# Performance work log

Hardware: AMD Instinct MI355X
Metric: run time of the kernel (lower is better)

The kernel has to match this reference:

```python
import jax, jax.numpy as jnp
import numpy as np

B, T, I, H, O = 128, 512, 256, 512, 256


def setup_inputs() -> dict:
    key = jax.random.key(0)
    ks = jax.random.split(key, 20)
    s_i = 1.0 / np.sqrt(I)
    s_h = 1.0 / np.sqrt(H)
    inp = {
        "x": jax.random.normal(ks[0], (B, T, I), dtype=jnp.float32),
        "Wix_w": jax.random.normal(ks[1], (H, I), dtype=jnp.float32) * s_i,
        "Wix_b": jax.random.normal(ks[2], (H,), dtype=jnp.float32) * s_i,
        "Wih_w": jax.random.normal(ks[3], (H, H), dtype=jnp.float32) * s_h,
        "Wih_b": jax.random.normal(ks[4], (H,), dtype=jnp.float32) * s_h,
        "bi": jnp.zeros((H,), dtype=jnp.float32),
        "Wfx_w": jax.random.normal(ks[5], (H, I), dtype=jnp.float32) * s_i,
        "Wfx_b": jax.random.normal(ks[6], (H,), dtype=jnp.float32) * s_i,
        "Wfh_w": jax.random.normal(ks[7], (H, H), dtype=jnp.float32) * s_h,
        "Wfh_b": jax.random.normal(ks[8], (H,), dtype=jnp.float32) * s_h,
        "bf": jnp.zeros((H,), dtype=jnp.float32),
        "Wgx_w": jax.random.normal(ks[9], (H, I), dtype=jnp.float32) * s_i,
        "Wgx_b": jax.random.normal(ks[10], (H,), dtype=jnp.float32) * s_i,
        "Wgh_w": jax.random.normal(ks[11], (H, H), dtype=jnp.float32) * s_h,
        "Wgh_b": jax.random.normal(ks[12], (H,), dtype=jnp.float32) * s_h,
        "bg": jnp.zeros((H,), dtype=jnp.float32),
        "Wox_w": jax.random.normal(ks[13], (H, I), dtype=jnp.float32) * s_i,
        "Wox_b": jax.random.normal(ks[14], (H,), dtype=jnp.float32) * s_i,
        "Woh_w": jax.random.normal(ks[15], (H, H), dtype=jnp.float32) * s_h,
        "Woh_b": jax.random.normal(ks[16], (H,), dtype=jnp.float32) * s_h,
        "bo": jnp.zeros((H,), dtype=jnp.float32),
        "Wph_w": jax.random.normal(ks[17], (O, H), dtype=jnp.float32) * s_h,
        "Wph_b": jax.random.normal(ks[18], (O,), dtype=jnp.float32) * s_h,
        "bp": jnp.zeros((O,), dtype=jnp.float32),
    }
    return inp


def reference(x, Wix_w, Wix_b, Wih_w, Wih_b, bi,
              Wfx_w, Wfx_b, Wfh_w, Wfh_b, bf,
              Wgx_w, Wgx_b, Wgh_w, Wgh_b, bg,
              Wox_w, Wox_b, Woh_w, Woh_b, bo,
              Wph_w, Wph_b, bp):
    batch = x.shape[0]
    h0 = jnp.zeros((batch, Wih_w.shape[0]), dtype=x.dtype)
    c0 = jnp.zeros_like(h0)

    # Precompute all input projections across time in 4 big GEMMs
    # (same math as per-step Linear calls, just batched over t).
    ix = jnp.einsum('bti,hi->bth', x, Wix_w) + Wix_b + bi
    fx = jnp.einsum('bti,hi->bth', x, Wfx_w) + Wfx_b + bf
    gx = jnp.einsum('bti,hi->bth', x, Wgx_w) + Wgx_b + bg
    ox = jnp.einsum('bti,hi->bth', x, Wox_w) + Wox_b + bo

    def step(carry, xt):
        h, c = carry
        ixt, fxt, gxt, oxt = xt
        i = jax.nn.sigmoid(ixt + h @ Wih_w.T + Wih_b)
        f = jax.nn.sigmoid(fxt + h @ Wfh_w.T + Wfh_b)
        g = jnp.tanh(gxt + h @ Wgh_w.T + Wgh_b)
        o = jax.nn.sigmoid(oxt + h @ Woh_w.T + Woh_b)
        c_new = g * i + c * f
        h_new = jnp.tanh(c_new) * o
        p = h_new @ Wph_w.T + Wph_b + bp
        y = jax.nn.softmax(p, axis=1)
        return (h_new, c_new), y

    # scan over time: [T, B, H] layout
    xs = (jnp.swapaxes(ix, 0, 1), jnp.swapaxes(fx, 0, 1),
          jnp.swapaxes(gx, 0, 1), jnp.swapaxes(ox, 0, 1))
    _, ys = jax.lax.scan(step, (h0, c0), xs)
    return jnp.swapaxes(ys, 0, 1)  # [B, T, O]
```

## Files before the change

kernel.cpp:

```cpp
#include <hip/hip_runtime.h>
#include <hip/hip_bf16.h>
#include <math.h>

#define B_  128
#define T_  512
#define I_  256
#define H_  512
#define O_  256
#define NP  2048
#define BT  65536
#define HB  65536

struct PrepArgs {
    const float* Whw[4];
    const float* Wxw[4];
    const float* Wxb[4];
    const float* Whb[4];
    const float* bg[4];
    const float* Wph_w;
    const float* Wph_b;
    const float* bp;
    float* Wt; float* Wg; float* WgT; float* WphT;
    float* xb; float* hb; float* pb;
};

#define PREP_TOTAL (1048576 + 524288 + 524288 + 131072 + 2048 + 2048 + 256)

__global__ __launch_bounds__(256) void k_prep(PrepArgs a) {
    int idx = blockIdx.x * 256 + threadIdx.x;
    if (idx >= PREP_TOTAL) return;
    int q = idx;
    if (q < 1048576) {
        int k = q >> 11, n = q & 2047;
        int g = n & 3, h = n >> 2;
        a.Wt[q] = a.Whw[g][h * H_ + k];
        return;
    }
    q -= 1048576;
    if (q < 524288) {
        int n = q >> 8, i = q & 255;
        int g = n & 3, h = n >> 2;
        a.Wg[q] = a.Wxw[g][h * I_ + i];
        return;
    }
    q -= 524288;
    if (q < 524288) {
        int i = q >> 11, n = q & 2047;
        int g = n & 3, h = n >> 2;
        a.WgT[q] = a.Wxw[g][h * I_ + i];
        return;
    }
    q -= 524288;
    if (q < 131072) {
        int h = q >> 8, o = q & 255;
        a.WphT[q] = a.Wph_w[o * H_ + h];
        return;
    }
    q -= 131072;
    if (q < 2048) {
        int g = q & 3, h = q >> 2;
        a.xb[q] = a.Wxb[g][h] + a.bg[g][h];
        return;
    }
    q -= 2048;
    if (q < 2048) {
        int g = q & 3, h = q >> 2;
        a.hb[q] = a.Whb[g][h];
        return;
    }
    q -= 2048;
    a.pb[q] = a.Wph_b[q] + a.bp[q];
}

__global__ __launch_bounds__(256) void k_transpose(const float* __restrict__ x,
                                                   float* __restrict__ xT2) {
    __shared__ float lds[32][33];
    int tid = threadIdx.x;
    int tx = tid & 31, ty = tid >> 5;
    int j0 = blockIdx.x * 32;
    int i0 = blockIdx.y * 32;
    int t  = j0 >> 7;
    int b0 = j0 & 127;
#pragma unroll
    for (int rr = 0; rr < 4; ++rr) {
        int jj = ty + rr * 8;
        lds[jj][tx] = x[((size_t)(b0 + jj) * T_ + t) * I_ + i0 + tx];
    }
    __syncthreads();
#pragma unroll
    for (int rr = 0; rr < 4; ++rr) {
        int ii = ty + rr * 8;
        xT2[(size_t)(i0 + ii) * BT + j0 + tx] = lds[tx][ii];
    }
}

__global__ __launch_bounds__(256, 1) void k_xgemm(const float* __restrict__ A,
                                                  const float* __restrict__ Bm,
                                                  const float* __restrict__ bias,
                                                  float* __restrict__ C) {
    __shared__ float As[16][128];
    __shared__ float Bs[16][128];
    int tid = threadIdx.x;
    int tx = tid & 15, ty = tid >> 4;
    int m0 = blockIdx.y * 128, j0 = blockIdx.x * 128;
    float acc[8][8];
#pragma unroll
    for (int i = 0; i < 8; ++i)
#pragma unroll
        for (int j = 0; j < 8; ++j) acc[i][j] = 0.f;

    for (int kt = 0; kt < I_; kt += 16) {
#pragma unroll
        for (int pp = 0; pp < 2; ++pp) {
            int p = tid + pp * 256;
            int row = p >> 2, kq = (p & 3) << 2;
            float4 av = *(const float4*)&A[(size_t)(m0 + row) * I_ + kt + kq];
            As[kq + 0][row] = av.x; As[kq + 1][row] = av.y;
            As[kq + 2][row] = av.z; As[kq + 3][row] = av.w;
        }
#pragma unroll
        for (int pp = 0; pp < 2; ++pp) {
            int p = tid + pp * 256;
            int krow = p >> 5, c4 = (p & 31) << 2;
            *(float4*)&Bs[krow][c4] =
                *(const float4*)&Bm[(size_t)(kt + krow) * BT + j0 + c4];
        }
        __syncthreads();
#pragma unroll
        for (int k = 0; k < 16; ++k) {
            float a[8], b[8];
            *(float4*)&a[0] = *(const float4*)&As[k][ty * 4];
            *(float4*)&a[4] = *(const float4*)&As[k][64 + ty * 4];
            *(float4*)&b[0] = *(const float4*)&Bs[k][tx * 4];
            *(float4*)&b[4] = *(const float4*)&Bs[k][64 + tx * 4];
#pragma unroll
            for (int i = 0; i < 8; ++i)
#pragma unroll
                for (int j = 0; j < 8; ++j) acc[i][j] += a[i] * b[j];
        }
        __syncthreads();
    }
#pragma unroll
    for (int i = 0; i < 8; ++i) {
        int mrow = (i < 4) ? (ty * 4 + i) : (64 + ty * 4 + (i - 4));
        int m = m0 + mrow;
        float bv = bias[m];
        float4 v0 = {acc[i][0] + bv, acc[i][1] + bv, acc[i][2] + bv, acc[i][3] + bv};
        float4 v1 = {acc[i][4] + bv, acc[i][5] + bv, acc[i][6] + bv, acc[i][7] + bv};
        *(float4*)&C[(size_t)m * BT + j0 + tx * 4] = v0;
        *(float4*)&C[(size_t)m * BT + j0 + 64 + tx * 4] = v1;
    }
}

__device__ inline float sigm(float v) { return 1.f / (1.f + expf(-v)); }

template <bool USE_XP>
__global__ __launch_bounds__(256, 1) void k_step(const float* __restrict__ Wt,
                                                 const float* __restrict__ WgT,
                                                 const float* __restrict__ xp,
                                                 const float* __restrict__ xT2,
                                                 const float* __restrict__ xb,
                                                 const float* __restrict__ hb,
                                                 float* __restrict__ hist,
                                                 float* __restrict__ cT,
                                                 int t) {
    __shared__ float red[4][16][64];
    int tid = threadIdx.x;
    int wave = tid >> 6, lane = tid & 63;
    int nt = blockIdx.x >> 1, bh = blockIdx.x & 1;
    int n0 = nt * 16, b0 = bh * 64;
    int b = b0 + lane;

    const float* hrow = hist + (size_t)t * HB;
    float acc[16];
#pragma unroll
    for (int j = 0; j < 16; ++j) acc[j] = 0.f;

    {
        int k0 = wave * 128;
        const float* hp = hrow + (size_t)k0 * B_ + b;
        const float* wp = Wt + (size_t)k0 * NP + n0;
        float hv[8];
#pragma unroll
        for (int u = 0; u < 8; ++u) hv[u] = hp[u * B_];
        for (int kb = 0; kb < 128; kb += 8) {
            float hn[8];
            if (kb + 8 < 128) {
                const float* hp2 = hp + (size_t)(kb + 8) * B_;
#pragma unroll
                for (int u = 0; u < 8; ++u) hn[u] = hp2[u * B_];
            }
#pragma unroll
            for (int u = 0; u < 8; ++u) {
                const float* w = wp + (size_t)(kb + u) * NP;
                float h0 = hv[u];
#pragma unroll
                for (int j = 0; j < 4; ++j) {
                    float4 wv = *(const float4*)(w + j * 4);
                    acc[j * 4 + 0] += h0 * wv.x;
                    acc[j * 4 + 1] += h0 * wv.y;
                    acc[j * 4 + 2] += h0 * wv.z;
                    acc[j * 4 + 3] += h0 * wv.w;
                }
            }
#pragma unroll
            for (int u = 0; u < 8; ++u) hv[u] = hn[u];
        }
    }
    if (!USE_XP) {
        int i0 = wave * 64;
        const float* xpp = xT2 + (size_t)i0 * BT + (size_t)t * B_ + b;
        const float* wp  = WgT + (size_t)i0 * NP + n0;
#pragma unroll 4
        for (int ii = 0; ii < 64; ++ii) {
            float xv = xpp[(size_t)ii * BT];
            const float* w = wp + (size_t)ii * NP;
#pragma unroll
            for (int j = 0; j < 4; ++j) {
                float4 wv = *(const float4*)(w + j * 4);
                acc[j * 4 + 0] += xv * wv.x;
                acc[j * 4 + 1] += xv * wv.y;
                acc[j * 4 + 2] += xv * wv.z;
                acc[j * 4 + 3] += xv * wv.w;
            }
        }
    }
#pragma unroll
    for (int j = 0; j < 16; ++j) red[wave][j][lane] = acc[j];
    __syncthreads();

    int b_l = tid & 63, h_i = tid >> 6;
    int n = n0 + h_i * 4;
    int h = nt * 4 + h_i;
    int bb = b0 + b_l;
    float pre[4];
#pragma unroll
    for (int g = 0; g < 4; ++g) {
        int j = h_i * 4 + g;
        pre[g] = red[0][j][b_l] + red[1][j][b_l] + red[2][j][b_l] + red[3][j][b_l];
        pre[g] += hb[n + g];
        if (USE_XP)
            pre[g] += xp[(size_t)(n + g) * BT + (size_t)t * B_ + bb];
        else
            pre[g] += xb[n + g];
    }
    float iv = sigm(pre[0]);
    float fv = sigm(pre[1]);
    float gv = tanhf(pre[2]);
    float ov = sigm(pre[3]);
    float c  = cT[h * B_ + bb];
    float cn = gv * iv + c * fv;
    cT[h * B_ + bb] = cn;
    hist[(size_t)(t + 1) * HB + h * B_ + bb] = tanhf(cn) * ov;
}

__global__ __launch_bounds__(256, 1) void k_outproj(const float* __restrict__ WphT,
                                                    const float* __restrict__ pb,
                                                    const float* __restrict__ hist,
                                                    float* __restrict__ pT) {
    __shared__ float red[4][16][64];
    int tid = threadIdx.x;
    int wave = tid >> 6, lane = tid & 63;
    int t = blockIdx.y;
    int ot = blockIdx.x >> 1, bh = blockIdx.x & 1;
    int o0 = ot * 16, b0 = bh * 64;
    int b = b0 + lane;

    const float* hrow = hist + (size_t)(t + 1) * HB;
    float acc[16];
#pragma unroll
    for (int j = 0; j < 16; ++j) acc[j] = 0.f;

    int k0 = wave * 128;
    const float* hp = hrow + (size_t)k0 * B_ + b;
    const float* wp = WphT + (size_t)k0 * O_ + o0;
    float hv[8];
#pragma unroll
    for (int u = 0; u < 8; ++u) hv[u] = hp[u * B_];
    for (int kb = 0; kb < 128; kb += 8) {
        float hn[8];
        if (kb + 8 < 128) {
            const float* hp2 = hp + (size_t)(kb + 8) * B_;
#pragma unroll
            for (int u = 0; u < 8; ++u) hn[u] = hp2[u * B_];
        }
#pragma unroll
        for (int u = 0; u < 8; ++u) {
            const float* w = wp + (size_t)(kb + u) * O_;
            float h0 = hv[u];
#pragma unroll
            for (int j = 0; j < 4; ++j) {
                float4 wv = *(const float4*)(w + j * 4);
                acc[j * 4 + 0] += h0 * wv.x;
                acc[j * 4 + 1] += h0 * wv.y;
                acc[j * 4 + 2] += h0 * wv.z;
                acc[j * 4 + 3] += h0 * wv.w;
            }
        }
#pragma unroll
        for (int u = 0; u < 8; ++u) hv[u] = hn[u];
    }
#pragma unroll
    for (int j = 0; j < 16; ++j) red[wave][j][lane] = acc[j];
    __syncthreads();

    int b_l = tid & 63, oi = tid >> 6;
    int bb = b0 + b_l;
#pragma unroll
    for (int g = 0; g < 4; ++g) {
        int j = oi * 4 + g;
        int o = o0 + j;
        float v = red[0][j][b_l] + red[1][j][b_l] + red[2][j][b_l] + red[3][j][b_l] + pb[o];
        pT[(size_t)t * (O_ * B_) + (size_t)o * B_ + bb] = v;
    }
}

__global__ __launch_bounds__(256, 1) void k_softmax(const float* __restrict__ pT,
                                                    float* __restrict__ out) {
    __shared__ float sm[32][257];
    __shared__ float rmax[32][8];
    __shared__ float rsum[32][8];
    int tid = threadIdx.x;
    int t = blockIdx.x >> 2, bq = blockIdx.x & 3;
    int b0 = bq * 32;
    const float* src = pT + (size_t)t * (O_ * B_);

#pragma unroll 4
    for (int it = 0; it < 32; ++it) {
        int idx = it * 256 + tid;
        int o = idx >> 5, b_l = idx & 31;
        sm[b_l][o] = src[(size_t)o * B_ + b0 + b_l];
    }
    __syncthreads();

    int b_l = tid >> 3, oc = tid & 7;
    float m = -3.4e38f;
#pragma unroll 4
    for (int oo = 0; oo < 32; ++oo) m = fmaxf(m, sm[b_l][oc * 32 + oo]);
    rmax[b_l][oc] = m;
    __syncthreads();
    float mm = rmax[b_l][0];
#pragma unroll
    for (int c = 1; c < 8; ++c) mm = fmaxf(mm, rmax[b_l][c]);

    float s = 0.f;
#pragma unroll 4
    for (int oo = 0; oo < 32; ++oo) s += expf(sm[b_l][oc * 32 + oo] - mm);
    rsum[b_l][oc] = s;
    __syncthreads();
    float st = 0.f;
#pragma unroll
    for (int c = 0; c < 8; ++c) st += rsum[b_l][c];
    float inv = 1.f / st;

    int bb = b0 + b_l;
    float* dst = out + ((size_t)bb * T_ + t) * O_ + oc * 32;
#pragma unroll 4
    for (int oo = 0; oo < 32; ++oo)
        dst[oo] = expf(sm[b_l][oc * 32 + oo] - mm) * inv;
}

extern "C" void kernel_launch(void* const* d_in, const int* in_sizes, int n_in,
                              void* d_out, int out_size, void* d_ws, size_t ws_size,
                              hipStream_t stream) {
    const float* x = (const float*)d_in[0];

    float* ws = (float*)d_ws;
    size_t off = 0;
    auto alloc = [&](size_t n) { float* p = ws + off; off += n; return p; };

    float* hist = alloc((size_t)513 * HB);
    float* cT   = alloc(HB);
    float* Wt   = alloc((size_t)512 * NP);
    float* Wg   = alloc((size_t)NP * I_);
    float* WgT  = alloc((size_t)I_ * NP);
    float* WphT = alloc((size_t)H_ * O_);
    float* xb   = alloc(NP);
    float* hb   = alloc(NP);
    float* pb   = alloc(O_);
    float* xT2  = alloc((size_t)I_ * BT);
    size_t baseBytes = off * sizeof(float);
    size_t xpBytes   = (size_t)NP * BT * sizeof(float);

    bool useXp = (ws_size >= baseBytes + xpBytes);
    float* xp = ws + off;
    float* pT = xT2;

    if (ws_size < baseBytes) return;

    hipMemsetAsync(hist, 0, HB * sizeof(float), stream);
    hipMemsetAsync(cT, 0, HB * sizeof(float), stream);

    PrepArgs pa;
    for (int g = 0; g < 4; ++g) {
        pa.Wxw[g] = (const float*)d_in[1 + 5 * g];
        pa.Wxb[g] = (const float*)d_in[2 + 5 * g];
        pa.Whw[g] = (const float*)d_in[3 + 5 * g];
        pa.Whb[g] = (const float*)d_in[4 + 5 * g];
        pa.bg[g]  = (const float*)d_in[5 + 5 * g];
    }
    pa.Wph_w = (const float*)d_in[21];
    pa.Wph_b = (const float*)d_in[22];
    pa.bp    = (const float*)d_in[23];
    pa.Wt = Wt; pa.Wg = Wg; pa.WgT = WgT; pa.WphT = WphT;
    pa.xb = xb; pa.hb = hb; pa.pb = pb;

    k_prep<<<(PREP_TOTAL + 255) / 256, 256, 0, stream>>>(pa);
    k_transpose<<<dim3(BT / 32, I_ / 32), 256, 0, stream>>>(x, xT2);

    if (useXp)
        k_xgemm<<<dim3(BT / 128, NP / 128), 256, 0, stream>>>(Wg, xT2, xb, xp);

    for (int t = 0; t < T_; ++t) {
        if (useXp)
            k_step<true><<<256, 256, 0, stream>>>(Wt, WgT, xp, xT2, xb, hb, hist, cT, t);
        else
            k_step<false><<<256, 256, 0, stream>>>(Wt, WgT, xp, xT2, xb, hb, hist, cT, t);
    }

    k_outproj<<<dim3(32, T_), 256, 0, stream>>>(WphT, pb, hist, pT);
    k_softmax<<<T_ * 4, 256, 0, stream>>>(pT, (float*)d_out);
}
```

Measured before the change: 17.03 ms.

## Replace per-timestep launches with persistent scan kernel using grid barrier

Swaps the 512 per-step kernel launches for one persistent kernel of 256 blocks. Blocks stay resident across time steps and synchronise through a global atomic counter per step. Each block's recurrent weight slice now lives in LDS, and the cell state is kept in registers instead of global memory. This removes launch overhead and repeated weight reloads from global memory, but relies on all 256 blocks being co-resident and on a spin barrier whose timeout could silently break correctness.

```diff
diff --git a/kernel.cpp b/kernel.cpp
--- a/kernel.cpp
+++ b/kernel.cpp
@@ -10,6 +10,7 @@
 #define NP  2048
 #define BT  65536
 #define HB  65536
+#define NBLK 256
 
 struct PrepArgs {
     const float* Whw[4];
@@ -155,103 +156,144 @@
 __device__ inline float sigm(float v) { return 1.f / (1.f + expf(-v)); }
 
 template <bool USE_XP>
-__global__ __launch_bounds__(256, 1) void k_step(const float* __restrict__ Wt,
+__global__ __launch_bounds__(512, 2) void k_scan(const float* __restrict__ Wt,
                                                  const float* __restrict__ WgT,
                                                  const float* __restrict__ xp,
                                                  const float* __restrict__ xT2,
                                                  const float* __restrict__ xb,
                                                  const float* __restrict__ hb,
                                                  float* __restrict__ hist,
-                                                 float* __restrict__ cT,
-                                                 int t) {
-    __shared__ float red[4][16][64];
+                                                 int* __restrict__ bar) {
+    __shared__ float wlds[512][16];
+    __shared__ float wxlds[256][16];
+    __shared__ float red[8][16][64];
+
     int tid = threadIdx.x;
     int wave = tid >> 6, lane = tid & 63;
     int nt = blockIdx.x >> 1, bh = blockIdx.x & 1;
     int n0 = nt * 16, b0 = bh * 64;
+
+    for (int p = tid; p < 2048; p += 512) {
+        int k = p >> 2, q = (p & 3) << 2;
+        *(float4*)&wlds[k][q] = *(const float4*)&Wt[(size_t)k * NP + n0 + q];
+    }
+    if (!USE_XP) {
+        for (int p = tid; p < 1024; p += 512) {
+            int i = p >> 2, q = (p & 3) << 2;
+            *(float4*)&wxlds[i][q] = *(const float4*)&WgT[(size_t)i * NP + n0 + q];
+        }
+    }
+
+    int h_i = tid >> 6, b_l = tid & 63;
+    float c_reg = 0.f;
+    float hbv[4] = {0, 0, 0, 0}, xbv[4] = {0, 0, 0, 0};
+    if (tid < 256) {
+#pragma unroll
+        for (int g = 0; g < 4; ++g) {
+            hbv[g] = hb[n0 + h_i * 4 + g];
+            if (!USE_XP) xbv[g] = xb[n0 + h_i * 4 + g];
+        }
+    }
+    __syncthreads();
+
     int b = b0 + lane;
-
-    const float* hrow = hist + (size_t)t * HB;
-    float acc[16];
-#pragma unroll
-    for (int j = 0; j < 16; ++j) acc[j] = 0.f;
-
-    {
-        int k0 = wave * 128;
-        const float* hp = hrow + (size_t)k0 * B_ + b;
-        const float* wp = Wt + (size_t)k0 * NP + n0;
+    int kc = wave * 64;
+
+    bool dead = false;
+    for (int t = 0; t < T_; ++t) {
+        const float* hp = hist + (size_t)t * HB + (size_t)kc * B_ + b;
+        float acc[16];
+#pragma unroll
+        for (int j = 0; j < 16; ++j) acc[j] = 0.f;
         float hv[8];
 #pragma unroll
         for (int u = 0; u < 8; ++u) hv[u] = hp[u * B_];
-        for (int kb = 0; kb < 128; kb += 8) {
+        for (int kb = 0; kb < 64; kb += 8) {
             float hn[8];
-            if (kb + 8 < 128) {
+            if (kb + 8 < 64) {
                 const float* hp2 = hp + (size_t)(kb + 8) * B_;
 #pragma unroll
                 for (int u = 0; u < 8; ++u) hn[u] = hp2[u * B_];
             }
 #pragma unroll
             for (int u = 0; u < 8; ++u) {
-                const float* w = wp + (size_t)(kb + u) * NP;
+                int k = kc + kb + u;
                 float h0 = hv[u];
 #pragma unroll
-                for (int j = 0; j < 4; ++j) {
-                    float4 wv = *(const float4*)(w + j * 4);
-                    acc[j * 4 + 0] += h0 * wv.x;
-                    acc[j * 4 + 1] += h0 * wv.y;
-                    acc[j * 4 + 2] += h0 * wv.z;
-                    acc[j * 4 + 3] += h0 * wv.w;
+                for (int j4 = 0; j4 < 4; ++j4) {
+                    float4 wv = *(const float4*)&wlds[k][j4 * 4];
+                    acc[j4 * 4 + 0] += h0 * wv.x;
+                    acc[j4 * 4 + 1] += h0 * wv.y;
+                    acc[j4 * 4 + 2] += h0 * wv.z;
+                    acc[j4 * 4 + 3] += h0 * wv.w;
                 }
             }
 #pragma unroll
             for (int u = 0; u < 8; ++u) hv[u] = hn[u];
         }
-    }
-    if (!USE_XP) {
-        int i0 = wave * 64;
-        const float* xpp = xT2 + (size_t)i0 * BT + (size_t)t * B_ + b;
-        const float* wp  = WgT + (size_t)i0 * NP + n0;
+        if (!USE_XP) {
+            int ic = wave * 32;
+            const float* xpp = xT2 + (size_t)ic * BT + (size_t)t * B_ + b;
 #pragma unroll 4
-        for (int ii = 0; ii < 64; ++ii) {
-            float xv = xpp[(size_t)ii * BT];
-            const float* w = wp + (size_t)ii * NP;
-#pragma unroll
-            for (int j = 0; j < 4; ++j) {
-                float4 wv = *(const float4*)(w + j * 4);
-                acc[j * 4 + 0] += xv * wv.x;
-                acc[j * 4 + 1] += xv * wv.y;
-                acc[j * 4 + 2] += xv * wv.z;
-                acc[j * 4 + 3] += xv * wv.w;
-            }
-        }
-    }
-#pragma unroll
-    for (int j = 0; j < 16; ++j) red[wave][j][lane] = acc[j];
-    __syncthreads();
-
-    int b_l = tid & 63, h_i = tid >> 6;
-    int n = n0 + h_i * 4;
-    int h = nt * 4 + h_i;
-    int bb = b0 + b_l;
-    float pre[4];
-#pragma unroll
-    for (int g = 0; g < 4; ++g) {
-        int j = h_i * 4 + g;
-        pre[g] = red[0][j][b_l] + red[1][j][b_l] + red[2][j][b_l] + red[3][j][b_l];
-        pre[g] += hb[n + g];
-        if (USE_XP)
-            pre[g] += xp[(size_t)(n + g) * BT + (size_t)t * B_ + bb];
-        else
-            pre[g] += xb[n + g];
-    }
-    float iv = sigm(pre[0]);
-    float fv = sigm(pre[1]);
-    float gv = tanhf(pre[2]);
-    float ov = sigm(pre[3]);
-    float c  = cT[h * B_ + bb];
-    float cn = gv * iv + c * fv;
-    cT[h * B_ + bb] = cn;
-    hist[(size_t)(t + 1) * HB + h * B_ + bb] = tanhf(cn) * ov;
+            for (int ii = 0; ii < 32; ++ii) {
+                float xv = xpp[(size_t)ii * BT];
+#pragma unroll
+                for (int j4 = 0; j4 < 4; ++j4) {
+                    float4 wv = *(const float4*)&wxlds[ic + ii][j4 * 4];
+                    acc[j4 * 4 + 0] += xv * wv.x;
+                    acc[j4 * 4 + 1] += xv * wv.y;
+                    acc[j4 * 4 + 2] += xv * wv.z;
+                    acc[j4 * 4 + 3] += xv * wv.w;
+                }
+            }
+        }
+#pragma unroll
+        for (int j = 0; j < 16; ++j) red[wave][j][lane] = acc[j];
+        __syncthreads();
+
+        if (tid < 256) {
+            float pre[4];
+#pragma unroll
+            for (int g = 0; g < 4; ++g) {
+                int j = h_i * 4 + g;
+                float s = red[0][j][b_l];
+#pragma unroll
+                for (int w = 1; w < 8; ++w) s += red[w][j][b_l];
+                pre[g] = s + hbv[g];
+            }
+            if (USE_XP) {
+#pragma unroll
+                for (int g = 0; g < 4; ++g)
+                    pre[g] += xp[(size_t)(n0 + h_i * 4 + g) * BT + (size_t)t * B_ + b0 + b_l];
+            } else {
+#pragma unroll
+                for (int g = 0; g < 4; ++g) pre[g] += xbv[g];
+            }
+            float iv = sigm(pre[0]);
+            float fv = sigm(pre[1]);
+            float gv = tanhf(pre[2]);
+            float ov = sigm(pre[3]);
+            c_reg = gv * iv + c_reg * fv;
+            hist[(size_t)(t + 1) * HB + (size_t)(nt * 4 + h_i) * B_ + b0 + b_l] =
+                tanhf(c_reg) * ov;
+        }
+        __syncthreads();
+
+        if (tid == 0) {
+            __hip_atomic_fetch_add(&bar[t], 1, __ATOMIC_RELEASE,
+                                   __HIP_MEMORY_SCOPE_AGENT);
+            if (!dead) {
+                int spins = 0;
+                while (__hip_atomic_load(&bar[t], __ATOMIC_RELAXED,
+                                         __HIP_MEMORY_SCOPE_AGENT) < NBLK) {
+                    __builtin_amdgcn_s_sleep(2);
+                    if (++spins > (1 << 20)) { dead = true; break; }
+                }
+            }
+        }
+        __syncthreads();
+        __builtin_amdgcn_fence(__ATOMIC_ACQUIRE, "agent");
+    }
 }
 
 __global__ __launch_bounds__(256, 1) void k_outproj(const float* __restrict__ WphT,
@@ -370,7 +412,6 @@
     auto alloc = [&](size_t n) { float* p = ws + off; off += n; return p; };
 
     float* hist = alloc((size_t)513 * HB);
-    float* cT   = alloc(HB);
     float* Wt   = alloc((size_t)512 * NP);
     float* Wg   = alloc((size_t)NP * I_);
     float* WgT  = alloc((size_t)I_ * NP);
@@ -378,6 +419,7 @@
     float* xb   = alloc(NP);
     float* hb   = alloc(NP);
     float* pb   = alloc(O_);
+    int*   bar  = (int*)alloc(512);
     float* xT2  = alloc((size_t)I_ * BT);
     size_t baseBytes = off * sizeof(float);
     size_t xpBytes   = (size_t)NP * BT * sizeof(float);
@@ -389,7 +431,7 @@
     if (ws_size < baseBytes) return;
 
     hipMemsetAsync(hist, 0, HB * sizeof(float), stream);
-    hipMemsetAsync(cT, 0, HB * sizeof(float), stream);
+    hipMemsetAsync(bar, 0, 512 * sizeof(int), stream);
 
     PrepArgs pa;
     for (int g = 0; g < 4; ++g) {
@@ -408,14 +450,11 @@
     k_prep<<<(PREP_TOTAL + 255) / 256, 256, 0, stream>>>(pa);
     k_transpose<<<dim3(BT / 32, I_ / 32), 256, 0, stream>>>(x, xT2);
 
-    if (useXp)
+    if (useXp) {
         k_xgemm<<<dim3(BT / 128, NP / 128), 256, 0, stream>>>(Wg, xT2, xb, xp);
-
-    for (int t = 0; t < T_; ++t) {
-        if (useXp)
-            k_step<true><<<256, 256, 0, stream>>>(Wt, WgT, xp, xT2, xb, hb, hist, cT, t);
-        else
-            k_step<false><<<256, 256, 0, stream>>>(Wt, WgT, xp, xT2, xb, hb, hist, cT, t);
+        k_scan<true><<<NBLK, 512, 0, stream>>>(Wt, WgT, xp, xT2, xb, hb, hist, bar);
+    } else {
+        k_scan<false><<<NBLK, 512, 0, stream>>>(Wt, WgT, xp, xT2, xb, hb, hist, bar);
     }
 
     k_outproj<<<dim3(32, T_), 256, 0, stream>>>(WphT, pb, hist, pT);
```

Result: no change. 17.31 ms (+1.6%).
